# Performance work log

Measured on AMD Instinct MI355X. Metric: run time of the kernel, lower is better.

## Reference

```python
import jax, jax.numpy as jnp
import numpy as np

B, C, H, W = 4, 512, 32, 32
NUM_HEADS, DIM_HEAD = 16, 32
DIM_ATTN = NUM_HEADS * DIM_HEAD  # 512
N = H * W


def setup_inputs() -> dict:
    key = jax.random.key(0)
    ks = jax.random.split(key, 6)
    s = 0.02
    return {
        "x": jax.random.normal(ks[0], (B, C, H, W), jnp.float32),
        "w_qkv": jax.random.normal(ks[1], (3 * DIM_ATTN, C), jnp.float32) * s,
        "b_qkv": jax.random.normal(ks[2], (3 * DIM_ATTN,), jnp.float32) * s,
        "w_proj": jax.random.normal(ks[3], (C, DIM_ATTN), jnp.float32) * s,
        "b_proj": jax.random.normal(ks[4], (C,), jnp.float32) * s,
        "shared_rel_pos": jax.random.normal(ks[5], (1, NUM_HEADS, N, N), jnp.float32) * s,
    }


def reference(x, w_qkv, b_qkv, w_proj, b_proj, shared_rel_pos):
    b, c, h, w = x.shape
    n = h * w
    scale = DIM_HEAD ** -0.5
    # 1x1 conv == per-pixel matmul over channels
    qkv = jnp.einsum('bchw,oc->bohw', x, w_qkv) + b_qkv[None, :, None, None]
    # [B, heads, 3*dh, N] -> chunk along dim 2 (matches torch .chunk(3, dim=2))
    qkv = qkv.reshape(b, NUM_HEADS, 3 * DIM_HEAD, n)
    q, k, v = jnp.split(qkv, 3, axis=2)          # each [B, heads, dh, N]
    attn = jnp.einsum('bhdi,bhdj->bhij', q, k) * scale  # q^T @ k
    attn = attn + shared_rel_pos
    attn = jax.nn.softmax(attn, axis=-1)
    out = jnp.einsum('bhdj,bhij->bhdi', v, attn)  # v @ attn^T, [B, heads, dh, N]
    out = out.reshape(b, NUM_HEADS * DIM_HEAD, h, w)
    out = jnp.einsum('bchw,oc->bohw', out, w_proj) + b_proj[None, :, None, None]
    return out
```

## Files before the change

kernel.cpp:

```cpp
#include <hip/hip_runtime.h>
#include <cstdint>
#include <cstddef>

#define BATCH 4
#define CIN   512
#define NPIX  1024
#define HEADS 16
#define DH    32
#define DATTN 512
#define O_QKV 1536

typedef unsigned short u16;
typedef __bf16 bf16x4 __attribute__((ext_vector_type(4)));
typedef __bf16 bf16x8 __attribute__((ext_vector_type(8)));
typedef float  f32x4  __attribute__((ext_vector_type(4)));

typedef const __attribute__((address_space(1))) void g1_t;
typedef __attribute__((address_space(3))) void l3_t;

#if defined(__has_builtin)
#if __has_builtin(__builtin_amdgcn_exp2f)
#define EXP2(x) __builtin_amdgcn_exp2f(x)
#endif
#endif
#ifndef EXP2
#define EXP2(x) __expf((x) * 0.6931471805599453f)
#endif

__device__ __forceinline__ u16 f2bf(float f) {
  unsigned u = __float_as_uint(f);
  u += 0x7fffu + ((u >> 16) & 1u);
  return (u16)(u >> 16);
}

__device__ __forceinline__ void gl_lds16(const void* gp, void* lp) {
  __builtin_amdgcn_global_load_lds((g1_t*)gp, (l3_t*)lp, 16, 0, 0);
}

__global__ __launch_bounds__(256) void prep_fused(const float* __restrict__ x,
                                                  const float* __restrict__ w1,
                                                  const float* __restrict__ w2,
                                                  u16* __restrict__ xt,
                                                  u16* __restrict__ o1,
                                                  u16* __restrict__ o2) {
  const int t = threadIdx.x;
  if (blockIdx.x < 512) {
    __shared__ float sT[64][65];
    const int q  = blockIdx.x;
    const int n0 = (q & 15) << 6;
    const int c0 = ((q >> 4) & 7) << 6;
    const int b  = q >> 7;
    const float* xb = x + ((size_t)b * CIN + c0) * NPIX + n0;
#pragma unroll
    for (int i = 0; i < 4; ++i) {
      int r   = i * 16 + (t >> 4);
      int col = (t & 15) << 2;
      float4 v = *reinterpret_cast<const float4*>(&xb[(size_t)r * NPIX + col]);
      sT[r][col + 0] = v.x; sT[r][col + 1] = v.y;
      sT[r][col + 2] = v.z; sT[r][col + 3] = v.w;
    }
    __syncthreads();
#pragma unroll
    for (int i = 0; i < 2; ++i) {
      int nl = t >> 2;
      int ch = (t & 3) + (i << 2);
      u16 tmp[8];
#pragma unroll
      for (int e = 0; e < 8; ++e) tmp[e] = f2bf(sT[(ch << 3) + e][nl]);
      *reinterpret_cast<uint4*>(&xt[((size_t)b * NPIX + n0 + nl) * CIN + c0 + (ch << 3)]) =
          *reinterpret_cast<uint4*>(tmp);
    }
  } else {
    const int idx = (blockIdx.x - 512) * 256 + t;
    const int n1 = (O_QKV * CIN) >> 2;
    float4 v = (idx < n1) ? reinterpret_cast<const float4*>(w1)[idx]
                          : reinterpret_cast<const float4*>(w2)[idx - n1];
    uint2 pk = make_uint2((unsigned)f2bf(v.x) | ((unsigned)f2bf(v.y) << 16),
                          (unsigned)f2bf(v.z) | ((unsigned)f2bf(v.w) << 16));
    if (idx < n1) reinterpret_cast<uint2*>(o1)[idx] = pk;
    else          reinterpret_cast<uint2*>(o2)[idx - n1] = pk;
  }
}

__global__ __launch_bounds__(256) void gemm_qkv_mfma(const u16* __restrict__ wq,
                                                     const u16* __restrict__ xt,
                                                     const float* __restrict__ bias,
                                                     u16* __restrict__ qt,
                                                     u16* __restrict__ kt,
                                                     u16* __restrict__ vt) {
  __shared__ __align__(16) u16 sA[96 * 64];
  __shared__ __align__(16) u16 sB[128 * 64];
  const int t  = threadIdx.x;
  const int w  = t >> 6, l = t & 63, g = l >> 4, ln = l & 15;
  const int n0 = blockIdx.x * 128;
  const int h  = blockIdx.y;
  const int b  = blockIdx.z;
  const int wm = w >> 1, wn = w & 1;

  const u16* wbase = wq + (size_t)h * 96 * CIN;
  const u16* xbase = xt + ((size_t)b * NPIX + n0) * CIN;

  f32x4 acc[3][4];
#pragma unroll
  for (int mi = 0; mi < 3; ++mi)
#pragma unroll
    for (int ni = 0; ni < 4; ++ni) acc[mi][ni] = {0.f, 0.f, 0.f, 0.f};

  for (int k0 = 0; k0 < CIN; k0 += 64) {
#pragma unroll
    for (int i = 0; i < 3; ++i) {
      int chunk = i * 256 + (w << 6) + l;
      gl_lds16(wbase + ((size_t)(chunk >> 3)) * CIN + k0 + ((chunk & 7) << 3),
               (char*)sA + i * 4096 + (w << 10));
    }
#pragma unroll
    for (int i = 0; i < 4; ++i) {
      int chunk = i * 256 + (w << 6) + l;
      gl_lds16(xbase + ((size_t)(chunk >> 3)) * CIN + k0 + ((chunk & 7) << 3),
               (char*)sB + i * 4096 + (w << 10));
    }
    __syncthreads();
#pragma unroll
    for (int kk = 0; kk < 64; kk += 32) {
      bf16x8 af[3], bfr[4];
#pragma unroll
      for (int mi = 0; mi < 3; ++mi)
        af[mi] = *reinterpret_cast<const bf16x8*>(&sA[(48 * wm + 16 * mi + ln) * 64 + kk + (g << 3)]);
#pragma unroll
      for (int ni = 0; ni < 4; ++ni)
        bfr[ni] = *reinterpret_cast<const bf16x8*>(&sB[((wn << 6) + (ni << 4) + ln) * 64 + kk + (g << 3)]);
#pragma unroll
      for (int mi = 0; mi < 3; ++mi)
#pragma unroll
        for (int ni = 0; ni < 4; ++ni)
          acc[mi][ni] = __builtin_amdgcn_mfma_f32_16x16x32_bf16(af[mi], bfr[ni], acc[mi][ni], 0, 0, 0);
    }
    __syncthreads();
  }

  const float QSC = 0.17677669529663687f * 1.4426950408889634f;
  const float* bh = bias + h * 96;
#pragma unroll
  for (int mi = 0; mi < 3; ++mi) {
    const int sec = 48 * wm + 16 * mi;
    const int rb  = sec + (g << 2);
    const float b0 = bh[rb + 0], b1 = bh[rb + 1], b2 = bh[rb + 2], b3 = bh[rb + 3];
#pragma unroll
    for (int ni = 0; ni < 4; ++ni) {
      const int n = n0 + (wn << 6) + (ni << 4) + ln;
      f32x4 a = acc[mi][ni];
      float v0 = a[0] + b0, v1 = a[1] + b1, v2 = a[2] + b2, v3 = a[3] + b3;
      if (sec < 32) { v0 *= QSC; v1 *= QSC; v2 *= QSC; v3 *= QSC; }
      u16 e0 = f2bf(v0), e1 = f2bf(v1), e2 = f2bf(v2), e3 = f2bf(v3);
      if (sec < 32) {
        const int d = sec + (g << 2);
        uint2 pk = make_uint2((unsigned)e0 | ((unsigned)e1 << 16),
                              (unsigned)e2 | ((unsigned)e3 << 16));
        *reinterpret_cast<uint2*>(&qt[(((size_t)(b * HEADS + h)) * NPIX + n) * DH + d]) = pk;
      } else if (sec < 64) {
        const int d = sec - 32 + (g << 2);
        uint2 pk = make_uint2((unsigned)e0 | ((unsigned)e1 << 16),
                              (unsigned)e2 | ((unsigned)e3 << 16));
        *reinterpret_cast<uint2*>(&kt[(((size_t)(b * HEADS + h)) * NPIX + n) * DH + d]) = pk;
      } else {
        const int d = sec - 64 + (g << 2);
        u16* vp = &vt[(((size_t)(b * HEADS + h)) * DH + d) * NPIX + n];
        vp[0] = e0; vp[NPIX] = e1; vp[2 * NPIX] = e2; vp[3 * NPIX] = e3;
      }
    }
  }
}

__global__ __launch_bounds__(256, 4) void attn_mfma(const u16* __restrict__ qt,
                                                    const u16* __restrict__ kt,
                                                    const u16* __restrict__ vt,
                                                    const float* __restrict__ rel,
                                                    u16* __restrict__ aout) {
  __shared__ __align__(16) u16 sK[2][4096];
  __shared__ __align__(16) u16 sV[2][4096];
  __shared__ __align__(16) u16 sP[4][2048];

  const int t  = threadIdx.x;
  const int w  = t >> 6, l = t & 63, g = l >> 4, ln = l & 15;
  const int bid = blockIdx.x;
  const int xcd = bid & 7, sl = bid >> 3;
  const int b   = sl & 3;
  const int i0  = ((sl >> 2) & 15) << 6;
  const int h   = (xcd << 1) | (sl >> 6);
  const int iw  = w;

  const size_t bh = (size_t)(b * HEADS + h);

  const int sc_r  = t >> 3;
  const int sc_kc = (t & 7) ^ (sc_r & 7) ^ ((sc_r >> 3) & 1);
  const int sc_vc = (t & 7) ^ (sc_r & 7);
  const u16* ksrc = kt + (bh * NPIX + ((sc_r << 1) | (sc_kc >> 2))) * DH +
                    ((sc_kc & 3) << 3);
  const u16* vsrc = vt + (bh * DH + sc_r) * NPIX + (sc_vc << 3);
  char* kdst = (char*)&sK[0][0] + (w << 10);
  char* vdst = (char*)&sV[0][0] + (w << 10);

#define STAGE(s_, p_) do {                                                  \
    gl_lds16(ksrc + (size_t)(s_) * 4096,        kdst + (p_) * 8192);        \
    gl_lds16(ksrc + (size_t)(s_) * 4096 + 2048, kdst + (p_) * 8192 + 4096); \
    gl_lds16(vsrc + (size_t)(s_) * 128,         vdst + (p_) * 8192);        \
    gl_lds16(vsrc + (size_t)(s_) * 128 + 64,    vdst + (p_) * 8192 + 4096); \
  } while (0)

  STAGE(0, 0);

  bf16x8 qf = *reinterpret_cast<const bf16x8*>(
      qt + (bh * NPIX + i0 + (iw << 4) + ln) * DH + (g << 3));

  const float* relp = rel + ((size_t)h * NPIX + i0 + (iw << 4) + (g << 2)) * NPIX +
                      (ln << 2);

  f32x4 vzero = {0.f, 0.f, 0.f, 0.f};
  f32x4 accO[2] = {vzero, vzero};
  f32x4 l_lane = vzero;

  u16* sPw = &sP[w][0];
  const float LOG2E = 1.4426950408889634f;

  for (int s = 0; s < 8; ++s) {
    const int p = s & 1;
    __syncthreads();
    if (s < 7) STAGE(s + 1, p ^ 1);

    f32x4 relv[2][4];
#pragma unroll
    for (int hh = 0; hh < 2; ++hh)
#pragma unroll
      for (int v = 0; v < 4; ++v)
        relv[hh][v] = *reinterpret_cast<const f32x4*>(
            relp + (size_t)v * NPIX + (s << 7) + (hh << 6));

    const u16* Kb = &sK[p][0];
    const u16* Vb = &sV[p][0];

    f32x4 sfr[8];
    __builtin_amdgcn_s_setprio(1);
#pragma unroll
    for (int jj = 0; jj < 8; ++jj) {
      const int hh = jj >> 2, q = jj & 3;
      const int r  = (ln << 1) + (q >> 1);
      const int ks = ((((q & 1) << 2) | g) ^ (r & 7)) ^ ((r >> 3) & 1);
      bf16x8 kf = *reinterpret_cast<const bf16x8*>(Kb + (hh << 11) + r * 64 + ks * 8);
      sfr[jj] = __builtin_amdgcn_mfma_f32_16x16x32_bf16(qf, kf, vzero, 0, 0, 0);
    }
    __builtin_amdgcn_s_setprio(0);

#pragma unroll
    for (int v = 0; v < 4; ++v) {
      const int rw = (g << 2) + v;
      const int pwoff = rw * 64 + ((((ln >> 1) ^ (rw & 7)) << 3) | ((ln & 1) << 2));
      float p0 = EXP2(fmaf(relv[0][v][0], LOG2E, sfr[0][v]));
      float p1 = EXP2(fmaf(relv[0][v][1], LOG2E, sfr[1][v]));
      float p2 = EXP2(fmaf(relv[0][v][2], LOG2E, sfr[2][v]));
      float p3 = EXP2(fmaf(relv[0][v][3], LOG2E, sfr[3][v]));
      l_lane[v] += (p0 + p1) + (p2 + p3);
      bf16x4 pk;
      pk[0] = (__bf16)p0; pk[1] = (__bf16)p1; pk[2] = (__bf16)p2; pk[3] = (__bf16)p3;
      *reinterpret_cast<bf16x4*>(sPw + pwoff) = pk;
      float p4 = EXP2(fmaf(relv[1][v][0], LOG2E, sfr[4][v]));
      float p5 = EXP2(fmaf(relv[1][v][1], LOG2E, sfr[5][v]));
      float p6 = EXP2(fmaf(relv[1][v][2], LOG2E, sfr[6][v]));
      float p7 = EXP2(fmaf(relv[1][v][3], LOG2E, sfr[7][v]));
      l_lane[v] += (p4 + p5) + (p6 + p7);
      bf16x4 pk2;
      pk2[0] = (__bf16)p4; pk2[1] = (__bf16)p5; pk2[2] = (__bf16)p6; pk2[3] = (__bf16)p7;
      *reinterpret_cast<bf16x4*>(sPw + 1024 + pwoff) = pk2;
    }

    __builtin_amdgcn_s_setprio(1);
#pragma unroll
    for (int c = 0; c < 4; ++c) {
      const int hh = c >> 1, kc2 = c & 1;
      const int lc = (kc2 << 2) | g;
      bf16x8 pa = *reinterpret_cast<const bf16x8*>(
          sPw + (hh << 10) + ln * 64 + ((lc ^ (ln & 7)) << 3));
#pragma unroll
      for (int dc = 0; dc < 2; ++dc) {
        const int d  = (dc << 4) + ln;
        const int vs = lc ^ (d & 7);
        bf16x8 vf = *reinterpret_cast<const bf16x8*>(Vb + (hh << 11) + d * 64 + vs * 8);
        accO[dc] = __builtin_amdgcn_mfma_f32_16x16x32_bf16(pa, vf, accO[dc], 0, 0, 0);
      }
    }
    __builtin_amdgcn_s_setprio(0);
  }
#undef STAGE

#pragma unroll
  for (int v = 0; v < 4; ++v) {
    float ls = l_lane[v];
    ls += __shfl_xor(ls, 1);
    ls += __shfl_xor(ls, 2);
    ls += __shfl_xor(ls, 4);
    ls += __shfl_xor(ls, 8);
    const float inv = 1.f / ls;
    const size_t row = (size_t)b * NPIX + i0 + (iw << 4) + (g << 2) + v;
    aout[row * DATTN + (h << 5) + ln]      = f2bf(accO[0][v] * inv);
    aout[row * DATTN + (h << 5) + 16 + ln] = f2bf(accO[1][v] * inv);
  }
}

__global__ __launch_bounds__(256) void gemm_proj_mfma(const u16* __restrict__ wp,
                                                      const u16* __restrict__ at,
                                                      const float* __restrict__ bias,
                                                      float* __restrict__ out) {
  __shared__ __align__(16) u16 sA[64 * 64];
  __shared__ __align__(16) u16 sB[128 * 64];
  const int t  = threadIdx.x;
  const int w  = t >> 6, l = t & 63, g = l >> 4, ln = l & 15;
  const int n0 = blockIdx.x * 128;
  const int o0 = blockIdx.y * 64;
  const int b  = blockIdx.z;
  const int wm = w >> 1, wn = w & 1;

  const u16* wbase = wp + (size_t)o0 * DATTN;
  const u16* abase = at + ((size_t)b * NPIX + n0) * DATTN;

  f32x4 acc[2][4];
#pragma unroll
  for (int mi = 0; mi < 2; ++mi)
#pragma unroll
    for (int ni = 0; ni < 4; ++ni) acc[mi][ni] = {0.f, 0.f, 0.f, 0.f};

  for (int k0 = 0; k0 < DATTN; k0 += 64) {
#pragma unroll
    for (int i = 0; i < 2; ++i) {
      int chunk = i * 256 + (w << 6) + l;
      gl_lds16(wbase + ((size_t)(chunk >> 3)) * DATTN + k0 + ((chunk & 7) << 3),
               (char*)sA + i * 4096 + (w << 10));
    }
#pragma unroll
    for (int i = 0; i < 4; ++i) {
      int chunk = i * 256 + (w << 6) + l;
      gl_lds16(abase + ((size_t)(chunk >> 3)) * DATTN + k0 + ((chunk & 7) << 3),
               (char*)sB + i * 4096 + (w << 10));
    }
    __syncthreads();
#pragma unroll
    for (int kk = 0; kk < 64; kk += 32) {
      bf16x8 af[2], bfr[4];
#pragma unroll
      for (int mi = 0; mi < 2; ++mi)
        af[mi] = *reinterpret_cast<const bf16x8*>(&sA[((wm << 5) + (mi << 4) + ln) * 64 + kk + (g << 3)]);
#pragma unroll
      for (int ni = 0; ni < 4; ++ni)
        bfr[ni] = *reinterpret_cast<const bf16x8*>(&sB[((wn << 6) + (ni << 4) + ln) * 64 + kk + (g << 3)]);
#pragma unroll
      for (int mi = 0; mi < 2; ++mi)
#pragma unroll
        for (int ni = 0; ni < 4; ++ni)
          acc[mi][ni] = __builtin_amdgcn_mfma_f32_16x16x32_bf16(af[mi], bfr[ni], acc[mi][ni], 0, 0, 0);
    }
    __syncthreads();
  }

#pragma unroll
  for (int mi = 0; mi < 2; ++mi) {
    const int o = o0 + (wm << 5) + (mi << 4) + (g << 2);
    const float b0 = bias[o], b1 = bias[o + 1], b2 = bias[o + 2], b3 = bias[o + 3];
#pragma unroll
    for (int ni = 0; ni < 4; ++ni) {
      const int n = n0 + (wn << 6) + (ni << 4) + ln;
      float* op = &out[((size_t)b * DATTN + o) * NPIX + n];
      op[0]        = acc[mi][ni][0] + b0;
      op[NPIX]     = acc[mi][ni][1] + b1;
      op[2 * NPIX] = acc[mi][ni][2] + b2;
      op[3 * NPIX] = acc[mi][ni][3] + b3;
    }
  }
}

extern "C" void kernel_launch(void* const* d_in, const int* in_sizes, int n_in,
                              void* d_out, int out_size, void* d_ws, size_t ws_size,
                              hipStream_t stream) {
  (void)in_sizes; (void)n_in; (void)out_size; (void)ws_size;
  const float* x      = (const float*)d_in[0];
  const float* w_qkv  = (const float*)d_in[1];
  const float* b_qkv  = (const float*)d_in[2];
  const float* w_proj = (const float*)d_in[3];
  const float* b_proj = (const float*)d_in[4];
  const float* rel    = (const float*)d_in[5];
  float* out = (float*)d_out;

  u16* xt    = (u16*)d_ws;
  u16* wq_bf = xt + (size_t)BATCH * NPIX * CIN;
  u16* wp_bf = wq_bf + (size_t)O_QKV * CIN;
  u16* qt    = wp_bf + (size_t)DATTN * DATTN;
  u16* kt    = qt + (size_t)BATCH * HEADS * NPIX * DH;
  u16* vt    = kt + (size_t)BATCH * HEADS * NPIX * DH;
  u16* aout  = vt + (size_t)BATCH * HEADS * NPIX * DH;

  prep_fused<<<1536, 256, 0, stream>>>(x, w_qkv, w_proj, xt, wq_bf, wp_bf);
  gemm_qkv_mfma<<<dim3(NPIX / 128, HEADS, BATCH), 256, 0, stream>>>(wq_bf, xt, b_qkv, qt, kt, vt);
  attn_mfma<<<1024, 256, 0, stream>>>(qt, kt, vt, rel, aout);
  gemm_proj_mfma<<<dim3(NPIX / 128, DATTN / 64, BATCH), 256, 0, stream>>>(wp_bf, aout, b_proj, out);
}
```

Measured before the change: 63.93 us.

## Pre-convert relative position bias to log2-scaled bf16 inside QKV GEMM launch

Adds extra blocks to the QKV GEMM launch that convert the fp32 relative-position bias to bf16, pre-multiplied by log2(e). The attention kernel then loads half-width bias values and skips the per-element multiply. The goal is to cut bias bandwidth in attention, where each head's bias is re-read once per batch. In exchange it adds a full extra read and write pass over the bias, plus bf16 rounding of the bias.

```diff
diff --git a/kernel.cpp b/kernel.cpp
--- a/kernel.cpp
+++ b/kernel.cpp
@@ -85,12 +85,33 @@
 __global__ __launch_bounds__(256) void gemm_qkv_mfma(const u16* __restrict__ wq,
                                                      const u16* __restrict__ xt,
                                                      const float* __restrict__ bias,
+                                                     const float* __restrict__ rel,
                                                      u16* __restrict__ qt,
                                                      u16* __restrict__ kt,
-                                                     u16* __restrict__ vt) {
+                                                     u16* __restrict__ vt,
+                                                     u16* __restrict__ relL) {
+  const int t = threadIdx.x;
+
+  if (blockIdx.x >= 8) {
+    const float LOG2E = 1.4426950408889634f;
+    const int c = (blockIdx.x - 8) + 32 * (blockIdx.y + 16 * blockIdx.z);
+    const size_t base = (size_t)c * 8192 + (size_t)t * 32;
+#pragma unroll
+    for (int i = 0; i < 4; ++i) {
+      f32x4 a = *reinterpret_cast<const f32x4*>(rel + base + i * 8);
+      f32x4 b4 = *reinterpret_cast<const f32x4*>(rel + base + i * 8 + 4);
+      u16 tmp[8];
+      tmp[0] = f2bf(a[0] * LOG2E);  tmp[1] = f2bf(a[1] * LOG2E);
+      tmp[2] = f2bf(a[2] * LOG2E);  tmp[3] = f2bf(a[3] * LOG2E);
+      tmp[4] = f2bf(b4[0] * LOG2E); tmp[5] = f2bf(b4[1] * LOG2E);
+      tmp[6] = f2bf(b4[2] * LOG2E); tmp[7] = f2bf(b4[3] * LOG2E);
+      *reinterpret_cast<uint4*>(relL + base + i * 8) = *reinterpret_cast<uint4*>(tmp);
+    }
+    return;
+  }
+
   __shared__ __align__(16) u16 sA[96 * 64];
   __shared__ __align__(16) u16 sB[128 * 64];
-  const int t  = threadIdx.x;
   const int w  = t >> 6, l = t & 63, g = l >> 4, ln = l & 15;
   const int n0 = blockIdx.x * 128;
   const int h  = blockIdx.y;
@@ -174,7 +195,7 @@
 __global__ __launch_bounds__(256, 4) void attn_mfma(const u16* __restrict__ qt,
                                                     const u16* __restrict__ kt,
                                                     const u16* __restrict__ vt,
-                                                    const float* __restrict__ rel,
+                                                    const u16* __restrict__ relL,
                                                     u16* __restrict__ aout) {
   __shared__ __align__(16) u16 sK[2][4096];
   __shared__ __align__(16) u16 sV[2][4096];
@@ -212,27 +233,26 @@
   bf16x8 qf = *reinterpret_cast<const bf16x8*>(
       qt + (bh * NPIX + i0 + (iw << 4) + ln) * DH + (g << 3));
 
-  const float* relp = rel + ((size_t)h * NPIX + i0 + (iw << 4) + (g << 2)) * NPIX +
-                      (ln << 2);
+  const u16* relp = relL + ((size_t)h * NPIX + i0 + (iw << 4) + (g << 2)) * NPIX +
+                    (ln << 2);
 
   f32x4 vzero = {0.f, 0.f, 0.f, 0.f};
   f32x4 accO[2] = {vzero, vzero};
   f32x4 l_lane = vzero;
 
   u16* sPw = &sP[w][0];
-  const float LOG2E = 1.4426950408889634f;
 
   for (int s = 0; s < 8; ++s) {
     const int p = s & 1;
     __syncthreads();
     if (s < 7) STAGE(s + 1, p ^ 1);
 
-    f32x4 relv[2][4];
+    uint2 relq[2][4];
 #pragma unroll
     for (int hh = 0; hh < 2; ++hh)
 #pragma unroll
       for (int v = 0; v < 4; ++v)
-        relv[hh][v] = *reinterpret_cast<const f32x4*>(
+        relq[hh][v] = *reinterpret_cast<const uint2*>(
             relp + (size_t)v * NPIX + (s << 7) + (hh << 6));
 
     const u16* Kb = &sK[p][0];
@@ -254,22 +274,36 @@
     for (int v = 0; v < 4; ++v) {
       const int rw = (g << 2) + v;
       const int pwoff = rw * 64 + ((((ln >> 1) ^ (rw & 7)) << 3) | ((ln & 1) << 2));
-      float p0 = EXP2(fmaf(relv[0][v][0], LOG2E, sfr[0][v]));
-      float p1 = EXP2(fmaf(relv[0][v][1], LOG2E, sfr[1][v]));
-      float p2 = EXP2(fmaf(relv[0][v][2], LOG2E, sfr[2][v]));
-      float p3 = EXP2(fmaf(relv[0][v][3], LOG2E, sfr[3][v]));
-      l_lane[v] += (p0 + p1) + (p2 + p3);
-      bf16x4 pk;
-      pk[0] = (__bf16)p0; pk[1] = (__bf16)p1; pk[2] = (__bf16)p2; pk[3] = (__bf16)p3;
-      *reinterpret_cast<bf16x4*>(sPw + pwoff) = pk;
-      float p4 = EXP2(fmaf(relv[1][v][0], LOG2E, sfr[4][v]));
-      float p5 = EXP2(fmaf(relv[1][v][1], LOG2E, sfr[5][v]));
-      float p6 = EXP2(fmaf(relv[1][v][2], LOG2E, sfr[6][v]));
-      float p7 = EXP2(fmaf(relv[1][v][3], LOG2E, sfr[7][v]));
-      l_lane[v] += (p4 + p5) + (p6 + p7);
-      bf16x4 pk2;
-      pk2[0] = (__bf16)p4; pk2[1] = (__bf16)p5; pk2[2] = (__bf16)p6; pk2[3] = (__bf16)p7;
-      *reinterpret_cast<bf16x4*>(sPw + 1024 + pwoff) = pk2;
+      {
+        const uint2 rq = relq[0][v];
+        float r0 = __uint_as_float((rq.x & 0xffffu) << 16);
+        float r1 = __uint_as_float(rq.x & 0xffff0000u);
+        float r2 = __uint_as_float((rq.y & 0xffffu) << 16);
+        float r3 = __uint_as_float(rq.y & 0xffff0000u);
+        float p0 = EXP2(r0 + sfr[0][v]);
+        float p1 = EXP2(r1 + sfr[1][v]);
+        float p2 = EXP2(r2 + sfr[2][v]);
+        float p3 = EXP2(r3 + sfr[3][v]);
+        l_lane[v] += (p0 + p1) + (p2 + p3);
+        bf16x4 pk;
+        pk[0] = (__bf16)p0; pk[1] = (__bf16)p1; pk[2] = (__bf16)p2; pk[3] = (__bf16)p3;
+        *reinterpret_cast<bf16x4*>(sPw + pwoff) = pk;
+      }
+      {
+        const uint2 rq = relq[1][v];
+        float r0 = __uint_as_float((rq.x & 0xffffu) << 16);
+        float r1 = __uint_as_float(rq.x & 0xffff0000u);
+        float r2 = __uint_as_float((rq.y & 0xffffu) << 16);
+        float r3 = __uint_as_float(rq.y & 0xffff0000u);
+        float p4 = EXP2(r0 + sfr[4][v]);
+        float p5 = EXP2(r1 + sfr[5][v]);
+        float p6 = EXP2(r2 + sfr[6][v]);
+        float p7 = EXP2(r3 + sfr[7][v]);
+        l_lane[v] += (p4 + p5) + (p6 + p7);
+        bf16x4 pk2;
+        pk2[0] = (__bf16)p4; pk2[1] = (__bf16)p5; pk2[2] = (__bf16)p6; pk2[3] = (__bf16)p7;
+        *reinterpret_cast<bf16x4*>(sPw + 1024 + pwoff) = pk2;
+      }
     }
 
     __builtin_amdgcn_s_setprio(1);
@@ -394,9 +428,11 @@
   u16* kt    = qt + (size_t)BATCH * HEADS * NPIX * DH;
   u16* vt    = kt + (size_t)BATCH * HEADS * NPIX * DH;
   u16* aout  = vt + (size_t)BATCH * HEADS * NPIX * DH;
+  u16* relL  = aout + (size_t)BATCH * NPIX * DATTN;
 
   prep_fused<<<1536, 256, 0, stream>>>(x, w_qkv, w_proj, xt, wq_bf, wp_bf);
-  gemm_qkv_mfma<<<dim3(NPIX / 128, HEADS, BATCH), 256, 0, stream>>>(wq_bf, xt, b_qkv, qt, kt, vt);
-  attn_mfma<<<1024, 256, 0, stream>>>(qt, kt, vt, rel, aout);
+  gemm_qkv_mfma<<<dim3(40, HEADS, BATCH), 256, 0, stream>>>(wq_bf, xt, b_qkv, rel,
+                                                            qt, kt, vt, relL);
+  attn_mfma<<<1024, 256, 0, stream>>>(qt, kt, vt, relL, aout);
   gemm_proj_mfma<<<dim3(NPIX / 128, DATTN / 64, BATCH), 256, 0, stream>>>(wp_bf, aout, b_proj, out);
 }
```

Result: slower. 81.83 us (+28.0%).
